# Performance work log

Hardware: AMD Instinct MI355X
Metric: run time of the kernel (lower is better)

## Reference

```python
import jax, jax.numpy as jnp
import numpy as np

B, TAU, D, DX, DZ, H = 512, 4, 5, 256, 16, 64
M = D * DZ
COEFF_KL = 1.0
LOG2PI = float(np.log(2.0 * np.pi))


def setup_inputs() -> dict:
    ks = jax.random.split(jax.random.key(0), 12)
    s = 0.05
    return {
        "x": jax.random.normal(ks[0], (B, TAU, D, DX), jnp.float32),
        "y": jax.random.normal(ks[1], (B, D, DX), jnp.float32),
        "mask_param": jnp.full((TAU, M, M), 5.0, jnp.float32),
        "w_enc": ((0.9 * jax.random.uniform(ks[2], (D, DZ, DX)) + 0.1) / DX).astype(jnp.float32),
        "w_dec": ((0.9 * jax.random.uniform(ks[3], (D, DX, DZ)) + 0.1) / DZ).astype(jnp.float32),
        "enc_W0": jax.random.normal(ks[4], (DZ, DX, H), jnp.float32) * s,
        "enc_b0": jnp.zeros((DZ, H), jnp.float32),
        "enc_W1": jax.random.normal(ks[5], (DZ, H), jnp.float32) * s,
        "enc_b1": jnp.zeros((DZ,), jnp.float32),
        "dec_W0": jax.random.normal(ks[6], (DX, DZ, H), jnp.float32) * s,
        "dec_b0": jnp.zeros((DX, H), jnp.float32),
        "dec_W1": jax.random.normal(ks[7], (DX, H), jnp.float32) * s,
        "dec_b1": jnp.zeros((DX,), jnp.float32),
        "t_W0": jax.random.normal(ks[8], (M, TAU * M, H), jnp.float32) * s,
        "t_b0": jnp.zeros((M, H), jnp.float32),
        "t_W1": jax.random.normal(ks[9], (M, H), jnp.float32) * s,
        "t_b1": jnp.zeros((M,), jnp.float32),
        "logvar_enc": jnp.full((D,), -1.0, jnp.float32),
        "logvar_dec": jnp.full((D,), -1.0, jnp.float32),
        "t_logvar": jnp.full((D, DZ), -4.0, jnp.float32),
    }


def _encode(x, w_enc, W0, b0, W1, b1):
    # x: (..., D, DX) -> mu: (..., D, DZ); d_z tiny MLPs gated by mixing weights
    masked = w_enc * x[..., None, :]  # (..., D, DZ, DX)
    h = jax.nn.leaky_relu(jnp.einsum('...ijx,jxh->...ijh', masked, W0) + b0)
    return jnp.einsum('...ijh,jh->...ij', h, W1) + b1


def _forward(x, y, mask_param, w_enc, w_dec, enc_W0, enc_b0, enc_W1, enc_b1,
             dec_W0, dec_b0, dec_W1, dec_b1, t_W0, t_b0, t_W1, t_b1,
             logvar_enc, logvar_dec, t_logvar):
    b = x.shape[0]
    k_adj, k_ep, k_et = jax.random.split(jax.random.key(42), 3)
    # gumbel-sigmoid soft adjacency sample (temperature 1, drawhard=False)
    u = jax.random.uniform(k_adj, (b, TAU, M, M), minval=1e-6, maxval=1.0 - 1e-6)
    adj = jax.nn.sigmoid(mask_param + jnp.log(u) - jnp.log1p(-u))  # (b,TAU,M,M)
    # encoder q(z|x): reparameterized gaussian, per-feature logvar
    q_std = jnp.exp(0.5 * logvar_enc)[:, None]                     # (D,1)
    mu_past = _encode(x, w_enc, enc_W0, enc_b0, enc_W1, enc_b1)    # (b,TAU,D,DZ)
    z_past = mu_past + q_std * jax.random.normal(k_ep, mu_past.shape, jnp.float32)
    mu_t = _encode(y, w_enc, enc_W0, enc_b0, enc_W1, enc_b1)       # (b,D,DZ)
    z_t = mu_t + q_std * jax.random.normal(k_et, mu_t.shape, jnp.float32)
    # transition p(z_t|z_<t): per-node MLP on adjacency-gated past latents
    zp = z_past.reshape(b, TAU, M)
    gated = adj * zp[:, :, None, :]                                # (b,TAU,node,src)
    gated = gated.transpose(0, 2, 1, 3).reshape(b, M, TAU * M)
    ht = jax.nn.leaky_relu(jnp.einsum('bmi,mih->bmh', gated, t_W0) + t_b0)
    pz_mu = (jnp.einsum('bmh,mh->bm', ht, t_W1) + t_b1).reshape(b, D, DZ)
    pz_std = jnp.exp(0.5 * t_logvar)                               # (D,DZ)
    # decoder p(x|z): d_x tiny MLPs on mixing-mask-gated latents
    masked_z = w_dec * z_t[:, :, None, :]                          # (b,D,DX,DZ)
    hd = jax.nn.leaky_relu(jnp.einsum('bijz,jzh->bijh', masked_z, dec_W0) + dec_b0)
    px_mu = jnp.einsum('bijh,jh->bij', hd, dec_W1) + dec_b1        # (b,D,DX)
    px_std = jnp.exp(0.5 * logvar_dec)[:, None]                    # (D,1)
    # ELBO: gaussian recon log-lik + analytic gaussian KL(q || p_transition)
    recon = -0.5 * ((y - px_mu) / px_std) ** 2 - jnp.log(px_std) - 0.5 * LOG2PI
    recon = recon.sum(axis=(1, 2)).mean()
    kl = (jnp.log(pz_std) - 0.5 * logvar_enc[:, None]
          + (q_std ** 2 + (mu_t - pz_mu) ** 2) / (2.0 * pz_std ** 2) - 0.5)
    kl = kl.sum(axis=(1, 2)).mean()
    return -(recon - COEFF_KL * kl)


def reference(x, y, mask_param, w_enc, w_dec, enc_W0, enc_b0, enc_W1, enc_b1,
              dec_W0, dec_b0, dec_W1, dec_b1, t_W0, t_b0, t_W1, t_b1,
              logvar_enc, logvar_dec, t_logvar):
    return _forward(x, y, mask_param, w_enc, w_dec, enc_W0, enc_b0, enc_W1, enc_b1,
                    dec_W0, dec_b0, dec_W1, dec_b1, t_W0, t_b0, t_W1, t_b1,
                    logvar_enc, logvar_dec, t_logvar)
```

## Files before the change

### kernel.cpp

```cpp
#include <hip/hip_runtime.h>
#include <cstdint>

constexpr int NB = 512, NTAU = 4, ND = 5, NDX = 256, NDZ = 16, NH = 64;
constexpr int NM  = ND * NDZ;
constexpr int NTM = NTAU * NM;
constexpr int NSAMP = NB * NTAU + NB;
constexpr float LOG2PI_F = 1.8378770664093453f;

typedef __attribute__((ext_vector_type(8))) short bf16x8;
typedef __attribute__((ext_vector_type(4))) float f32x4;

__device__ __forceinline__ unsigned long long mix64(unsigned long long z) {
  z += 0x9E3779B97F4A7C15ull;
  z = (z ^ (z >> 30)) * 0xBF58476D1CE4E5B9ull;
  z = (z ^ (z >> 27)) * 0x94D049BB133111EBull;
  return z ^ (z >> 31);
}
__device__ __forceinline__ float u01f(unsigned long long h) {
  return ((float)(unsigned)(h >> 40) + 0.5f) * (1.0f / 16777216.0f);
}
__device__ __forceinline__ float rng_normal(unsigned long long salt, unsigned long long idx) {
  float u1 = u01f(mix64(salt + 2ull * idx));
  float u2 = u01f(mix64(salt + 2ull * idx + 1ull));
  float r = sqrtf(-2.0f * logf(u1));
  return r * cosf(6.283185307179586f * u2);
}
constexpr unsigned long long SALT_ADJ = 0x1000000000000ull;
constexpr unsigned long long SALT_EP  = 0x2000000000000ull;
constexpr unsigned long long SALT_ET  = 0x3000000000000ull;

__device__ __forceinline__ short f2bf(float f) {
  unsigned u = __float_as_uint(f);
  unsigned r = (u + 0x7FFFu + ((u >> 16) & 1u)) >> 16;
  return (short)r;
}

__global__ __launch_bounds__(256) void k_prepW(
    const float* __restrict__ y,
    const float* __restrict__ w_enc, const float* __restrict__ eW0, short* __restrict__ PtE,
    const float* __restrict__ w_dec, const float* __restrict__ dW0, short* __restrict__ QtD,
    const float* __restrict__ mask_param, float* __restrict__ em,
    const float* __restrict__ tW0, short* __restrict__ TtB,
    float* __restrict__ yT)
{
  __shared__ short lds[64][65];
  const int bid = blockIdx.x;
  if (bid < 640) {
    int e0 = (bid * 256 + threadIdx.x) * 8;
    int d = e0 / (1024 * NDX);
    int r = e0 % (1024 * NDX);
    int col = r >> 8, x0 = r & 255;
    int z = col >> 6, h = col & 63;
    const float* wep = &w_enc[((size_t)d * NDZ + z) * NDX + x0];
    float4 w0 = *(const float4*)wep;
    float4 w1 = *(const float4*)(wep + 4);
    const float* w0base = &eW0[((size_t)z * NDX + x0) * NH + h];
    bf16x8 o;
    o[0] = f2bf(w0.x * w0base[0 * NH]); o[1] = f2bf(w0.y * w0base[1 * NH]);
    o[2] = f2bf(w0.z * w0base[2 * NH]); o[3] = f2bf(w0.w * w0base[3 * NH]);
    o[4] = f2bf(w1.x * w0base[4 * NH]); o[5] = f2bf(w1.y * w0base[5 * NH]);
    o[6] = f2bf(w1.z * w0base[6 * NH]); o[7] = f2bf(w1.w * w0base[7 * NH]);
    *(bf16x8*)&PtE[e0] = o;
  } else if (bid < 960) {
    int t = (bid - 640) * 256 + threadIdx.x;
    int d = t / (NDX * NH);
    int r = t % (NDX * NH);
    int xx = r >> 6, h = r & 63;
    size_t base = (size_t)t * 32;
    #pragma unroll
    for (int z = 0; z < NDZ; ++z)
      QtD[base + z] = f2bf(w_dec[((size_t)d * NDX + xx) * NDZ + z] *
                           dW0[((size_t)xx * NDZ + z) * NH + h]);
    #pragma unroll
    for (int z = NDZ; z < 32; ++z) QtD[base + z] = 0;
  } else if (bid < 1060) {
    int idx = (bid - 960) * 256 + threadIdx.x;
    em[idx] = expf(-mask_param[idx]);
  } else if (bid < 1460) {
    int r = bid - 1060;
    int kt = r % 5, m = r / 5;
    int k0 = kt * 64;
    for (int idx = threadIdx.x; idx < 64 * 64; idx += 256) {
      int hh = idx & 63, kk = idx >> 6;
      lds[kk][hh] = f2bf(tW0[((size_t)m * NTM + k0 + kk) * NH + hh]);
    }
    __syncthreads();
    for (int idx = threadIdx.x; idx < 64 * 64; idx += 256) {
      int kk = idx & 63, hh = idx >> 6;
      TtB[((size_t)m * NH + hh) * NTM + k0 + kk] = lds[kk][hh];
    }
  } else {
    int e0 = ((bid - 1460) * 256 + threadIdx.x) * 4;
    int d = e0 / (NDX * NB);
    int rem = e0 % (NDX * NB);
    int xx = rem >> 9, b0 = rem & 511;
    float4 o;
    o.x = y[((size_t)(b0 + 0) * ND + d) * NDX + xx];
    o.y = y[((size_t)(b0 + 1) * ND + d) * NDX + xx];
    o.z = y[((size_t)(b0 + 2) * ND + d) * NDX + xx];
    o.w = y[((size_t)(b0 + 3) * ND + d) * NDX + xx];
    *(float4*)&yT[e0] = o;
  }
}

__global__ __launch_bounds__(512) void k_enc_mfma(
    const float* __restrict__ x, const float* __restrict__ y,
    const short* __restrict__ PtE,
    const float* __restrict__ b0, const float* __restrict__ W1,
    const float* __restrict__ b1, const float* __restrict__ lve,
    float* __restrict__ z_past, float* __restrict__ mu_t, float* __restrict__ z_t)
{
  __shared__ __align__(16) short Bs[64 * 264];
  __shared__ float mu_s[128][4];

  const int d = blockIdx.z, zq = blockIdx.y;
  const int s0 = blockIdx.x * 128;
  const int tid = threadIdx.x;
  const int w = tid >> 6, l = tid & 63;
  const int lrow = l & 15, g = l >> 4;

  const int srow = s0 + w * 16 + lrow;
  const float* Asrc = (srow < NB * NTAU)
      ? &x[((size_t)srow * ND + d) * NDX]
      : &y[((size_t)(srow - NB * NTAU) * ND + d) * NDX];
  bf16x8 a[8];
  #pragma unroll
  for (int ks = 0; ks < 8; ++ks) {
    const float* p = Asrc + g * 8 + ks * 32;
    float4 f0 = *(const float4*)p;
    float4 f1 = *(const float4*)(p + 4);
    a[ks][0] = f2bf(f0.x); a[ks][1] = f2bf(f0.y);
    a[ks][2] = f2bf(f0.z); a[ks][3] = f2bf(f0.w);
    a[ks][4] = f2bf(f1.x); a[ks][5] = f2bf(f1.y);
    a[ks][6] = f2bf(f1.z); a[ks][7] = f2bf(f1.w);
  }

  const int stg_row = tid >> 3;
  const int stg_c   = (tid & 7) * 32;

  for (int zi = 0; zi < 4; ++zi) {
    const int z = zq * 4 + zi;
    {
      const short* src = PtE + ((size_t)(d * 1024 + z * 64 + stg_row)) * NDX + stg_c;
      short* dst = Bs + stg_row * 264 + stg_c;
      #pragma unroll
      for (int j = 0; j < 4; ++j)
        *(bf16x8*)(dst + j * 8) = *(const bf16x8*)(src + j * 8);
    }
    __syncthreads();

    f32x4 acc[4] = {};
    #pragma unroll
    for (int nt = 0; nt < 4; ++nt) {
      const short* Brow = Bs + (nt * 16 + lrow) * 264 + g * 8;
      #pragma unroll
      for (int ks = 0; ks < 8; ++ks) {
        bf16x8 bv = *(const bf16x8*)(Brow + ks * 32);
        acc[nt] = __builtin_amdgcn_mfma_f32_16x16x32_bf16(a[ks], bv, acc[nt], 0, 0, 0);
      }
    }

    float b0v[4], w1v[4];
    #pragma unroll
    for (int nt = 0; nt < 4; ++nt) {
      int h = nt * 16 + lrow;
      b0v[nt] = b0[z * NH + h];
      w1v[nt] = W1[z * NH + h];
    }
    const float b1v = b1[z];
    #pragma unroll
    for (int reg = 0; reg < 4; ++reg) {
      float v = 0.0f;
      #pragma unroll
      for (int nt = 0; nt < 4; ++nt) {
        float hv = acc[nt][reg] + b0v[nt];
        hv = fmaxf(hv, 0.01f * hv);
        v += hv * w1v[nt];
      }
      #pragma unroll
      for (int off = 1; off < 16; off <<= 1) v += __shfl_xor(v, off, 16);
      if (lrow == 0)
        mu_s[w * 16 + g * 4 + reg][zi] = v + b1v;
    }
    __syncthreads();
  }

  {
    const int sl = tid >> 2, zi = tid & 3;
    const int z = zq * 4 + zi;
    const int s = s0 + sl;
    const int m = d * NDZ + z;
    float mu = mu_s[sl][zi];
    float qs = expf(0.5f * lve[d]);
    if (s < NB * NTAU) {
      float eps = rng_normal(SALT_EP, (unsigned long long)s * NM + m);
      z_past[(size_t)s * NM + m] = mu + qs * eps;
    } else {
      int b = s - NB * NTAU;
      float eps = rng_normal(SALT_ET, (unsigned long long)b * NM + m);
      size_t o = (size_t)b * NM + m;
      mu_t[o] = mu;
      z_t[o]  = mu + qs * eps;
    }
  }
}

__global__ __launch_bounds__(512) void k_tail(
    const float* __restrict__ em, const float* __restrict__ z_past,
    const short* __restrict__ TtB,
    const float* __restrict__ tb0, const float* __restrict__ tW1,
    const float* __restrict__ tb1, const float* __restrict__ lve,
    const float* __restrict__ t_logvar, const float* __restrict__ mu_t,
    float* __restrict__ kl_partial,
    const float* __restrict__ zt, const short* __restrict__ QtD,
    const float* __restrict__ yT, const float* __restrict__ db0,
    const float* __restrict__ dW1, const float* __restrict__ db1,
    const float* __restrict__ lvd, float* __restrict__ rec_partial)
{
  __shared__ __align__(16) short Bls[64 * 328];
  __shared__ float ems[NTM];
  __shared__ float redb[8];

  const int bid = blockIdx.x;
  const int tid = threadIdx.x;

  if (bid < 320) {
    const int m = bid >> 2;
    const int b0 = (bid & 3) * 128;
    const int w = tid >> 6, l = tid & 63;
    const int lrow = l & 15, g = l >> 4;

    for (int i = tid; i < NTM; i += 512) {
      int t = i / NM, s = i - t * NM;
      ems[i] = em[(t * NM + m) * NM + s];
    }
    {
      const int r = tid >> 3;
      const int c0 = (tid & 7) * 40;
      const short* src = TtB + ((size_t)(m * NH + r)) * NTM + c0;
      short* dst = Bls + r * 328 + c0;
      #pragma unroll
      for (int j = 0; j < 5; ++j)
        *(bf16x8*)(dst + j * 8) = *(const bf16x8*)(src + j * 8);
    }
    __syncthreads();

    const int brow = b0 + w * 16 + lrow;
    const float* zrow = z_past + (size_t)brow * NTM;
    bf16x8 a[10];
    #pragma unroll
    for (int ks = 0; ks < 10; ++ks) {
      const int tm0 = g * 8 + ks * 32;
      const int t = tm0 / NM;
      const int s0 = tm0 - t * NM;
      unsigned long long aibase =
          ((unsigned long long)((brow * NTAU + t) * NM + m)) * NM + s0;
      unsigned long long h0 = mix64(SALT_ADJ + aibase);
      unsigned long long h1 = mix64(SALT_ADJ + aibase + 2);
      unsigned long long h2 = mix64(SALT_ADJ + aibase + 4);
      unsigned long long h3 = mix64(SALT_ADJ + aibase + 6);
      float u[8];
      u[0] = ((float)(unsigned)(h0 >> 40) + 0.5f) * (1.0f / 16777216.0f);
      u[1] = ((float)((unsigned)(h0 >> 16) & 0xFFFFFFu) + 0.5f) * (1.0f / 16777216.0f);
      u[2] = ((float)(unsigned)(h1 >> 40) + 0.5f) * (1.0f / 16777216.0f);
      u[3] = ((float)((unsigned)(h1 >> 16) & 0xFFFFFFu) + 0.5f) * (1.0f / 16777216.0f);
      u[4] = ((float)(unsigned)(h2 >> 40) + 0.5f) * (1.0f / 16777216.0f);
      u[5] = ((float)((unsigned)(h2 >> 16) & 0xFFFFFFu) + 0.5f) * (1.0f / 16777216.0f);
      u[6] = ((float)(unsigned)(h3 >> 40) + 0.5f) * (1.0f / 16777216.0f);
      u[7] = ((float)((unsigned)(h3 >> 16) & 0xFFFFFFu) + 0.5f) * (1.0f / 16777216.0f);
      float4 z0 = *(const float4*)(zrow + tm0);
      float4 z1 = *(const float4*)(zrow + tm0 + 4);
      const float* zvp0 = &z0.x;
      const float* zvp1 = &z1.x;
      #pragma unroll
      for (int j = 0; j < 8; ++j) {
        float uu = fminf(fmaxf(u[j], 1e-6f), 1.0f - 1e-6f);
        float e = ems[tm0 + j];
        float den = fmaf(e, 1.0f - uu, uu);
        float adj = uu * __builtin_amdgcn_rcpf(den);
        float zv = (j < 4) ? zvp0[j] : zvp1[j - 4];
        a[ks][j] = f2bf(adj * zv);
      }
    }

    f32x4 acc[4] = {};
    #pragma unroll
    for (int nt = 0; nt < 4; ++nt) {
      const short* Brow = Bls + (nt * 16 + lrow) * 328 + g * 8;
      #pragma unroll
      for (int ks = 0; ks < 10; ++ks) {
        bf16x8 bv = *(const bf16x8*)(Brow + ks * 32);
        acc[nt] = __builtin_amdgcn_mfma_f32_16x16x32_bf16(a[ks], bv, acc[nt], 0, 0, 0);
      }
    }

    float b0v[4], w1v[4];
    #pragma unroll
    for (int nt = 0; nt < 4; ++nt) {
      int h = nt * 16 + lrow;
      b0v[nt] = tb0[m * NH + h];
      w1v[nt] = tW1[m * NH + h];
    }

    const int d = m >> 4;
    const float lv_t = t_logvar[m];
    const float lv_e = lve[d];
    const float inv2var = 0.5f * expf(-lv_t);
    const float qvar = expf(lv_e);
    const float cterm = 0.5f * lv_t - 0.5f * lv_e - 0.5f;
    const float bv1 = tb1[m];

    float klw = 0.0f;
    #pragma unroll
    for (int reg = 0; reg < 4; ++reg) {
      float v = 0.0f;
      #pragma unroll
      for (int nt = 0; nt < 4; ++nt) {
        float hv = acc[nt][reg] + b0v[nt];
        hv = fmaxf(hv, 0.01f * hv);
        v += hv * w1v[nt];
      }
      #pragma unroll
      for (int off = 1; off < 16; off <<= 1) v += __shfl_xor(v, off, 16);
      if (lrow == 0) {
        int b = b0 + w * 16 + g * 4 + reg;
        float pz = v + bv1;
        float diff = mu_t[(size_t)b * NM + m] - pz;
        klw += cterm + (qvar + diff * diff) * inv2var;
      }
    }
    klw += __shfl_xor(klw, 16, 64);
    klw += __shfl_xor(klw, 32, 64);

    if (l == 0) redb[w] = klw;
    __syncthreads();
    if (tid == 0) {
      float s = 0.f;
      #pragma unroll
      for (int i = 0; i < 8; ++i) s += redb[i];
      kl_partial[(bid & 3) * NM + m] = s;
    }
  } else {
    const int idx = bid - 320;
    const int d = idx >> 8, xx = idx & 255;
    const int w8 = tid >> 6, l = tid & 63;
    const int mb = w8 >> 2, w = w8 & 3;
    const int lrow = l & 15, g = l >> 4;

    bf16x8 bfr[4];
    const short* Bbase = QtD + ((size_t)((d * NDX + xx) * NH)) * 32;
    #pragma unroll
    for (int nt = 0; nt < 4; ++nt)
      bfr[nt] = *(const bf16x8*)(Bbase + (nt * 16 + lrow) * 32 + g * 8);

    f32x4 acc[4][4] = {};
    #pragma unroll
    for (int mt = 0; mt < 4; ++mt) {
      int b = mb * 256 + w * 64 + mt * 16 + lrow;
      bf16x8 a = {0, 0, 0, 0, 0, 0, 0, 0};
      if (g < 2) {
        const float* zp = zt + (size_t)b * NM + d * NDZ + g * 8;
        float4 f0 = *(const float4*)zp;
        float4 f1 = *(const float4*)(zp + 4);
        a[0] = f2bf(f0.x); a[1] = f2bf(f0.y); a[2] = f2bf(f0.z); a[3] = f2bf(f0.w);
        a[4] = f2bf(f1.x); a[5] = f2bf(f1.y); a[6] = f2bf(f1.z); a[7] = f2bf(f1.w);
      }
      #pragma unroll
      for (int nt = 0; nt < 4; ++nt)
        acc[mt][nt] = __builtin_amdgcn_mfma_f32_16x16x32_bf16(a, bfr[nt], acc[mt][nt], 0, 0, 0);
    }

    float db0v[4], dW1v[4];
    #pragma unroll
    for (int nt = 0; nt < 4; ++nt) {
      int h = nt * 16 + lrow;
      db0v[nt] = db0[xx * NH + h];
      dW1v[nt] = dW1[xx * NH + h];
    }
    const float lv = lvd[d];
    const float inv_std = expf(-0.5f * lv);
    const float cterm = -0.5f * lv - 0.5f * LOG2PI_F;
    const float b1v = db1[xx];

    float racc = 0.0f;
    #pragma unroll
    for (int mt = 0; mt < 4; ++mt) {
      float rs[4];
      #pragma unroll
      for (int reg = 0; reg < 4; ++reg) {
        float v = 0.0f;
        #pragma unroll
        for (int nt = 0; nt < 4; ++nt) {
          float hv = acc[mt][nt][reg] + db0v[nt];
          hv = fmaxf(hv, 0.01f * hv);
          v += hv * dW1v[nt];
        }
        #pragma unroll
        for (int off = 1; off < 16; off <<= 1) v += __shfl_xor(v, off, 16);
        rs[reg] = v;
      }
      if (lrow == 0) {
        int b = mb * 256 + w * 64 + mt * 16 + g * 4;
        float4 yv = *(const float4*)&yT[((size_t)d * NDX + xx) * NB + b];
        const float* yvp = &yv.x;
        #pragma unroll
        for (int reg = 0; reg < 4; ++reg) {
          float px = rs[reg] + b1v;
          float e = (yvp[reg] - px) * inv_std;
          racc += -0.5f * e * e + cterm;
        }
      }
    }
    racc += __shfl_xor(racc, 16, 64);
    racc += __shfl_xor(racc, 32, 64);

    if (l == 0) redb[w8] = racc;
    __syncthreads();
    if (tid == 0) {
      float s = 0.f;
      #pragma unroll
      for (int i = 0; i < 8; ++i) s += redb[i];
      rec_partial[(size_t)d * NDX + xx] = s;
    }
  }
}

__global__ __launch_bounds__(256) void k_reduce(
    const float* __restrict__ rp, const float* __restrict__ kp,
    float* __restrict__ out)
{
  __shared__ float sr[4], sk[4];
  float r = 0.f, k = 0.f;
  for (int i = threadIdx.x; i < 1280; i += 256) r += rp[i];
  for (int i = threadIdx.x; i < 320; i += 256) k += kp[i];
  #pragma unroll
  for (int off = 32; off; off >>= 1) {
    r += __shfl_xor(r, off, 64);
    k += __shfl_xor(k, off, 64);
  }
  int wv = threadIdx.x >> 6;
  if ((threadIdx.x & 63) == 0) { sr[wv] = r; sk[wv] = k; }
  __syncthreads();
  if (threadIdx.x == 0) {
    float R = sr[0] + sr[1] + sr[2] + sr[3];
    float K = sk[0] + sk[1] + sk[2] + sk[3];
    out[0] = (K - R) / (float)NB;
  }
}

extern "C" void kernel_launch(void* const* d_in, const int* in_sizes, int n_in,
                              void* d_out, int out_size, void* d_ws, size_t ws_size,
                              hipStream_t stream) {
  (void)in_sizes; (void)n_in; (void)out_size; (void)ws_size;
  const float* x        = (const float*)d_in[0];
  const float* y        = (const float*)d_in[1];
  const float* mask_p   = (const float*)d_in[2];
  const float* w_enc    = (const float*)d_in[3];
  const float* w_dec    = (const float*)d_in[4];
  const float* enc_W0   = (const float*)d_in[5];
  const float* enc_b0   = (const float*)d_in[6];
  const float* enc_W1   = (const float*)d_in[7];
  const float* enc_b1   = (const float*)d_in[8];
  const float* dec_W0   = (const float*)d_in[9];
  const float* dec_b0   = (const float*)d_in[10];
  const float* dec_W1   = (const float*)d_in[11];
  const float* dec_b1   = (const float*)d_in[12];
  const float* t_W0     = (const float*)d_in[13];
  const float* t_b0     = (const float*)d_in[14];
  const float* t_W1     = (const float*)d_in[15];
  const float* t_b1     = (const float*)d_in[16];
  const float* lv_enc   = (const float*)d_in[17];
  const float* lv_dec   = (const float*)d_in[18];
  const float* t_logvar = (const float*)d_in[19];

  float* ws     = (float*)d_ws;
  float* z_past = ws;
  float* mu_t   = z_past + 163840;
  float* z_t    = mu_t + 40960;
  float* rec_p  = z_t + 40960;
  float* kl_p   = rec_p + 1280;
  float* em     = kl_p + 320;
  float* yTb    = em + 25600;
  short* PtE    = (short*)(yTb + 655360);
  short* QtD    = PtE + 5 * 1024 * NDX;
  short* TtB    = QtD + 5 * NDX * NH * 32;

  k_prepW<<<2100, 256, 0, stream>>>(
      y, w_enc, enc_W0, PtE, w_dec, dec_W0, QtD, mask_p, em, t_W0, TtB, yTb);

  k_enc_mfma<<<dim3(NSAMP / 128, 4, ND), 512, 0, stream>>>(
      x, y, PtE, enc_b0, enc_W1, enc_b1, lv_enc, z_past, mu_t, z_t);
  k_tail<<<1600, 512, 0, stream>>>(
      em, z_past, TtB, t_b0, t_W1, t_b1, lv_enc, t_logvar, mu_t, kl_p,
      z_t, QtD, yTb, dec_b0, dec_W1, dec_b1, lv_dec, rec_p);
  k_reduce<<<1, 256, 0, stream>>>(rec_p, kl_p, (float*)d_out);
}
```

Baseline: 72.44 us.

## Fuse weight preparation into encoder kernel and compute mask exp inline in tail

Merges the separate weight-prep kernel into the encoder kernel. Encoder blocks now build the w_enc-scaled bf16 weight tile directly in LDS from enc_W0 instead of reading a precomputed PtE buffer, and the other prep jobs (decoder weights, transition weight transpose, y transpose) run as extra blocks of the same launch. exp(-mask_param) is computed inline in the tail kernel, so the em buffer goes away. This removes one kernel launch and the PtE round trip through global memory. In exchange, each encoder block redoes the weight scaling and reads enc_W0 with strided fp32 loads, and that work is repeated across the 20 sample tiles.

```diff
diff --git a/kernel.cpp b/kernel.cpp
--- a/kernel.cpp
+++ b/kernel.cpp
@@ -35,34 +35,132 @@
   return (short)r;
 }
 
-__global__ __launch_bounds__(256) void k_prepW(
-    const float* __restrict__ y,
-    const float* __restrict__ w_enc, const float* __restrict__ eW0, short* __restrict__ PtE,
-    const float* __restrict__ w_dec, const float* __restrict__ dW0, short* __restrict__ QtD,
-    const float* __restrict__ mask_param, float* __restrict__ em,
+__global__ __launch_bounds__(512) void k_enc_mfma(
+    const float* __restrict__ x, const float* __restrict__ y,
+    const float* __restrict__ w_enc, const float* __restrict__ eW0,
+    const float* __restrict__ b0, const float* __restrict__ W1,
+    const float* __restrict__ b1, const float* __restrict__ lve,
+    float* __restrict__ z_past, float* __restrict__ mu_t, float* __restrict__ z_t,
+    const float* __restrict__ w_dec, const float* __restrict__ dW0,
+    short* __restrict__ QtD,
     const float* __restrict__ tW0, short* __restrict__ TtB,
     float* __restrict__ yT)
 {
-  __shared__ short lds[64][65];
+  __shared__ __align__(16) char smem[40448];
   const int bid = blockIdx.x;
-  if (bid < 640) {
-    int e0 = (bid * 256 + threadIdx.x) * 8;
-    int d = e0 / (1024 * NDX);
-    int r = e0 % (1024 * NDX);
-    int col = r >> 8, x0 = r & 255;
-    int z = col >> 6, h = col & 63;
-    const float* wep = &w_enc[((size_t)d * NDZ + z) * NDX + x0];
-    float4 w0 = *(const float4*)wep;
-    float4 w1 = *(const float4*)(wep + 4);
-    const float* w0base = &eW0[((size_t)z * NDX + x0) * NH + h];
-    bf16x8 o;
-    o[0] = f2bf(w0.x * w0base[0 * NH]); o[1] = f2bf(w0.y * w0base[1 * NH]);
-    o[2] = f2bf(w0.z * w0base[2 * NH]); o[3] = f2bf(w0.w * w0base[3 * NH]);
-    o[4] = f2bf(w1.x * w0base[4 * NH]); o[5] = f2bf(w1.y * w0base[5 * NH]);
-    o[6] = f2bf(w1.z * w0base[6 * NH]); o[7] = f2bf(w1.w * w0base[7 * NH]);
-    *(bf16x8*)&PtE[e0] = o;
-  } else if (bid < 960) {
-    int t = (bid - 640) * 256 + threadIdx.x;
+  const int tid = threadIdx.x;
+
+  if (bid < 400) {
+    short* Bs     = (short*)smem;
+    float* wenc_s = (float*)(smem + 33792);
+    float (*mu_s)[4] = (float(*)[4])(smem + 37888);
+
+    const int d = bid / 80;
+    const int r80 = bid % 80;
+    const int zq = r80 / 20;
+    const int s0 = (r80 % 20) * 128;
+    const int w = tid >> 6, l = tid & 63;
+    const int lrow = l & 15, g = l >> 4;
+
+    for (int i = tid; i < 4 * NDX; i += 512) {
+      int zi = i >> 8, k = i & 255;
+      wenc_s[i] = w_enc[((size_t)d * NDZ + zq * 4 + zi) * NDX + k];
+    }
+
+    const int srow = s0 + w * 16 + lrow;
+    const float* Asrc = (srow < NB * NTAU)
+        ? &x[((size_t)srow * ND + d) * NDX]
+        : &y[((size_t)(srow - NB * NTAU) * ND + d) * NDX];
+    bf16x8 a[8];
+    #pragma unroll
+    for (int ks = 0; ks < 8; ++ks) {
+      const float* p = Asrc + g * 8 + ks * 32;
+      float4 f0 = *(const float4*)p;
+      float4 f1 = *(const float4*)(p + 4);
+      a[ks][0] = f2bf(f0.x); a[ks][1] = f2bf(f0.y);
+      a[ks][2] = f2bf(f0.z); a[ks][3] = f2bf(f0.w);
+      a[ks][4] = f2bf(f1.x); a[ks][5] = f2bf(f1.y);
+      a[ks][6] = f2bf(f1.z); a[ks][7] = f2bf(f1.w);
+    }
+    __syncthreads();
+
+    const int c  = tid >> 3;
+    const int kc = (tid & 7) * 32;
+
+    for (int zi = 0; zi < 4; ++zi) {
+      const int z = zq * 4 + zi;
+      {
+        const float* ep = eW0 + ((size_t)z * NDX + kc) * NH + c;
+        short* dst = Bs + c * 264 + kc;
+        #pragma unroll
+        for (int jb = 0; jb < 4; ++jb) {
+          bf16x8 o;
+          #pragma unroll
+          for (int j = 0; j < 8; ++j) {
+            float v = wenc_s[zi * 256 + kc + jb * 8 + j] * ep[(jb * 8 + j) * NH];
+            o[j] = f2bf(v);
+          }
+          *(bf16x8*)(dst + jb * 8) = o;
+        }
+      }
+      __syncthreads();
+
+      f32x4 acc[4] = {};
+      #pragma unroll
+      for (int nt = 0; nt < 4; ++nt) {
+        const short* Brow = Bs + (nt * 16 + lrow) * 264 + g * 8;
+        #pragma unroll
+        for (int ks = 0; ks < 8; ++ks) {
+          bf16x8 bv = *(const bf16x8*)(Brow + ks * 32);
+          acc[nt] = __builtin_amdgcn_mfma_f32_16x16x32_bf16(a[ks], bv, acc[nt], 0, 0, 0);
+        }
+      }
+
+      float b0v[4], w1v[4];
+      #pragma unroll
+      for (int nt = 0; nt < 4; ++nt) {
+        int h = nt * 16 + lrow;
+        b0v[nt] = b0[z * NH + h];
+        w1v[nt] = W1[z * NH + h];
+      }
+      const float b1v = b1[z];
+      #pragma unroll
+      for (int reg = 0; reg < 4; ++reg) {
+        float v = 0.0f;
+        #pragma unroll
+        for (int nt = 0; nt < 4; ++nt) {
+          float hv = acc[nt][reg] + b0v[nt];
+          hv = fmaxf(hv, 0.01f * hv);
+          v += hv * w1v[nt];
+        }
+        #pragma unroll
+        for (int off = 1; off < 16; off <<= 1) v += __shfl_xor(v, off, 16);
+        if (lrow == 0)
+          mu_s[w * 16 + g * 4 + reg][zi] = v + b1v;
+      }
+      __syncthreads();
+    }
+
+    {
+      const int sl = tid >> 2, zi = tid & 3;
+      const int z = zq * 4 + zi;
+      const int s = s0 + sl;
+      const int m = d * NDZ + z;
+      float mu = mu_s[sl][zi];
+      float qs = expf(0.5f * lve[d]);
+      if (s < NB * NTAU) {
+        float eps = rng_normal(SALT_EP, (unsigned long long)s * NM + m);
+        z_past[(size_t)s * NM + m] = mu + qs * eps;
+      } else {
+        int b = s - NB * NTAU;
+        float eps = rng_normal(SALT_ET, (unsigned long long)b * NM + m);
+        size_t o = (size_t)b * NM + m;
+        mu_t[o] = mu;
+        z_t[o]  = mu + qs * eps;
+      }
+    }
+  } else if (bid < 560) {
+    int t = (bid - 400) * 512 + tid;
     int d = t / (NDX * NH);
     int r = t % (NDX * NH);
     int xx = r >> 6, h = r & 63;
@@ -73,140 +171,36 @@
                            dW0[((size_t)xx * NDZ + z) * NH + h]);
     #pragma unroll
     for (int z = NDZ; z < 32; ++z) QtD[base + z] = 0;
-  } else if (bid < 1060) {
-    int idx = (bid - 960) * 256 + threadIdx.x;
-    em[idx] = expf(-mask_param[idx]);
-  } else if (bid < 1460) {
-    int r = bid - 1060;
+  } else if (bid < 960) {
+    short (*lds)[65] = (short(*)[65])smem;
+    int r = bid - 560;
     int kt = r % 5, m = r / 5;
     int k0 = kt * 64;
-    for (int idx = threadIdx.x; idx < 64 * 64; idx += 256) {
+    for (int idx = tid; idx < 64 * 64; idx += 512) {
       int hh = idx & 63, kk = idx >> 6;
       lds[kk][hh] = f2bf(tW0[((size_t)m * NTM + k0 + kk) * NH + hh]);
     }
     __syncthreads();
-    for (int idx = threadIdx.x; idx < 64 * 64; idx += 256) {
+    for (int idx = tid; idx < 64 * 64; idx += 512) {
       int kk = idx & 63, hh = idx >> 6;
       TtB[((size_t)m * NH + hh) * NTM + k0 + kk] = lds[kk][hh];
     }
   } else {
-    int e0 = ((bid - 1460) * 256 + threadIdx.x) * 4;
+    int e0 = ((bid - 960) * 512 + tid) * 4;
     int d = e0 / (NDX * NB);
     int rem = e0 % (NDX * NB);
-    int xx = rem >> 9, b0 = rem & 511;
+    int xx = rem >> 9, b0i = rem & 511;
     float4 o;
-    o.x = y[((size_t)(b0 + 0) * ND + d) * NDX + xx];
-    o.y = y[((size_t)(b0 + 1) * ND + d) * NDX + xx];
-    o.z = y[((size_t)(b0 + 2) * ND + d) * NDX + xx];
-    o.w = y[((size_t)(b0 + 3) * ND + d) * NDX + xx];
+    o.x = y[((size_t)(b0i + 0) * ND + d) * NDX + xx];
+    o.y = y[((size_t)(b0i + 1) * ND + d) * NDX + xx];
+    o.z = y[((size_t)(b0i + 2) * ND + d) * NDX + xx];
+    o.w = y[((size_t)(b0i + 3) * ND + d) * NDX + xx];
     *(float4*)&yT[e0] = o;
   }
 }
 
-__global__ __launch_bounds__(512) void k_enc_mfma(
-    const float* __restrict__ x, const float* __restrict__ y,
-    const short* __restrict__ PtE,
-    const float* __restrict__ b0, const float* __restrict__ W1,
-    const float* __restrict__ b1, const float* __restrict__ lve,
-    float* __restrict__ z_past, float* __restrict__ mu_t, float* __restrict__ z_t)
-{
-  __shared__ __align__(16) short Bs[64 * 264];
-  __shared__ float mu_s[128][4];
-
-  const int d = blockIdx.z, zq = blockIdx.y;
-  const int s0 = blockIdx.x * 128;
-  const int tid = threadIdx.x;
-  const int w = tid >> 6, l = tid & 63;
-  const int lrow = l & 15, g = l >> 4;
-
-  const int srow = s0 + w * 16 + lrow;
-  const float* Asrc = (srow < NB * NTAU)
-      ? &x[((size_t)srow * ND + d) * NDX]
-      : &y[((size_t)(srow - NB * NTAU) * ND + d) * NDX];
-  bf16x8 a[8];
-  #pragma unroll
-  for (int ks = 0; ks < 8; ++ks) {
-    const float* p = Asrc + g * 8 + ks * 32;
-    float4 f0 = *(const float4*)p;
-    float4 f1 = *(const float4*)(p + 4);
-    a[ks][0] = f2bf(f0.x); a[ks][1] = f2bf(f0.y);
-    a[ks][2] = f2bf(f0.z); a[ks][3] = f2bf(f0.w);
-    a[ks][4] = f2bf(f1.x); a[ks][5] = f2bf(f1.y);
-    a[ks][6] = f2bf(f1.z); a[ks][7] = f2bf(f1.w);
-  }
-
-  const int stg_row = tid >> 3;
-  const int stg_c   = (tid & 7) * 32;
-
-  for (int zi = 0; zi < 4; ++zi) {
-    const int z = zq * 4 + zi;
-    {
-      const short* src = PtE + ((size_t)(d * 1024 + z * 64 + stg_row)) * NDX + stg_c;
-      short* dst = Bs + stg_row * 264 + stg_c;
-      #pragma unroll
-      for (int j = 0; j < 4; ++j)
-        *(bf16x8*)(dst + j * 8) = *(const bf16x8*)(src + j * 8);
-    }
-    __syncthreads();
-
-    f32x4 acc[4] = {};
-    #pragma unroll
-    for (int nt = 0; nt < 4; ++nt) {
-      const short* Brow = Bs + (nt * 16 + lrow) * 264 + g * 8;
-      #pragma unroll
-      for (int ks = 0; ks < 8; ++ks) {
-        bf16x8 bv = *(const bf16x8*)(Brow + ks * 32);
-        acc[nt] = __builtin_amdgcn_mfma_f32_16x16x32_bf16(a[ks], bv, acc[nt], 0, 0, 0);
-      }
-    }
-
-    float b0v[4], w1v[4];
-    #pragma unroll
-    for (int nt = 0; nt < 4; ++nt) {
-      int h = nt * 16 + lrow;
-      b0v[nt] = b0[z * NH + h];
-      w1v[nt] = W1[z * NH + h];
-    }
-    const float b1v = b1[z];
-    #pragma unroll
-    for (int reg = 0; reg < 4; ++reg) {
-      float v = 0.0f;
-      #pragma unroll
-      for (int nt = 0; nt < 4; ++nt) {
-        float hv = acc[nt][reg] + b0v[nt];
-        hv = fmaxf(hv, 0.01f * hv);
-        v += hv * w1v[nt];
-      }
-      #pragma unroll
-      for (int off = 1; off < 16; off <<= 1) v += __shfl_xor(v, off, 16);
-      if (lrow == 0)
-        mu_s[w * 16 + g * 4 + reg][zi] = v + b1v;
-    }
-    __syncthreads();
-  }
-
-  {
-    const int sl = tid >> 2, zi = tid & 3;
-    const int z = zq * 4 + zi;
-    const int s = s0 + sl;
-    const int m = d * NDZ + z;
-    float mu = mu_s[sl][zi];
-    float qs = expf(0.5f * lve[d]);
-    if (s < NB * NTAU) {
-      float eps = rng_normal(SALT_EP, (unsigned long long)s * NM + m);
-      z_past[(size_t)s * NM + m] = mu + qs * eps;
-    } else {
-      int b = s - NB * NTAU;
-      float eps = rng_normal(SALT_ET, (unsigned long long)b * NM + m);
-      size_t o = (size_t)b * NM + m;
-      mu_t[o] = mu;
-      z_t[o]  = mu + qs * eps;
-    }
-  }
-}
-
 __global__ __launch_bounds__(512) void k_tail(
-    const float* __restrict__ em, const float* __restrict__ z_past,
+    const float* __restrict__ mask_param, const float* __restrict__ z_past,
     const short* __restrict__ TtB,
     const float* __restrict__ tb0, const float* __restrict__ tW1,
     const float* __restrict__ tb1, const float* __restrict__ lve,
@@ -232,7 +226,7 @@
 
     for (int i = tid; i < NTM; i += 512) {
       int t = i / NM, s = i - t * NM;
-      ems[i] = em[(t * NM + m) * NM + s];
+      ems[i] = expf(-mask_param[(t * NM + m) * NM + s]);
     }
     {
       const int r = tid >> 3;
@@ -479,19 +473,15 @@
   float* z_t    = mu_t + 40960;
   float* rec_p  = z_t + 40960;
   float* kl_p   = rec_p + 1280;
-  float* em     = kl_p + 320;
-  float* yTb    = em + 25600;
-  short* PtE    = (short*)(yTb + 655360);
-  short* QtD    = PtE + 5 * 1024 * NDX;
+  float* yTb    = kl_p + 320;
+  short* QtD    = (short*)(yTb + 655360);
   short* TtB    = QtD + 5 * NDX * NH * 32;
 
-  k_prepW<<<2100, 256, 0, stream>>>(
-      y, w_enc, enc_W0, PtE, w_dec, dec_W0, QtD, mask_p, em, t_W0, TtB, yTb);
-
-  k_enc_mfma<<<dim3(NSAMP / 128, 4, ND), 512, 0, stream>>>(
-      x, y, PtE, enc_b0, enc_W1, enc_b1, lv_enc, z_past, mu_t, z_t);
+  k_enc_mfma<<<1280, 512, 0, stream>>>(
+      x, y, w_enc, enc_W0, enc_b0, enc_W1, enc_b1, lv_enc,
+      z_past, mu_t, z_t, w_dec, dec_W0, QtD, t_W0, TtB, yTb);
   k_tail<<<1600, 512, 0, stream>>>(
-      em, z_past, TtB, t_b0, t_W1, t_b1, lv_enc, t_logvar, mu_t, kl_p,
+      mask_p, z_past, TtB, t_b0, t_W1, t_b1, lv_enc, t_logvar, mu_t, kl_p,
       z_t, QtD, yTb, dec_b0, dec_W1, dec_b1, lv_dec, rec_p);
   k_reduce<<<1, 256, 0, stream>>>(rec_p, kl_p, (float*)d_out);
 }
```

Result: slower. 85.41 us (+17.9%).
